# Optimization experiments

Measured on AMD Instinct MI355X. Metric: run time of the kernel, lower is better.

Reference implementation:

```python
import jax, jax.numpy as jnp
import numpy as np
from jax import lax

BETA = 0.95
THRESH = 1.0
NUM_INPUTS, NUM_HIDDEN, NUM_CLASSES, NUM_STEPS, BATCH = 80, 256, 2, 200, 4096


@jax.custom_vjp
def spike_fn(x):
    # Heaviside spike; surrogate gradient = fast_sigmoid (slope=25)
    return (x > 0).astype(x.dtype)

def _spike_fwd(x):
    return spike_fn(x), x

def _spike_bwd(x, g):
    slope = 25.0
    return (g / (slope * jnp.abs(x) + 1.0) ** 2,)

spike_fn.defvjp(_spike_fwd, _spike_bwd)


def _linear_init(key, fan_in, fan_out):
    # torch nn.Linear default init: U(-1/sqrt(fan_in), 1/sqrt(fan_in))
    k1, k2 = jax.random.split(key)
    bound = 1.0 / np.sqrt(fan_in)
    W = jax.random.uniform(k1, (fan_out, fan_in), jnp.float32, -bound, bound)
    b = jax.random.uniform(k2, (fan_out,), jnp.float32, -bound, bound)
    return W, b


def setup_inputs() -> dict:
    key = jax.random.key(0)
    kx, k1, k2, k3, k4 = jax.random.split(key, 5)
    x = jax.random.normal(kx, (BATCH, NUM_INPUTS, NUM_STEPS), jnp.float32)
    W1, b1 = _linear_init(k1, NUM_INPUTS, NUM_HIDDEN)
    W2, b2 = _linear_init(k2, NUM_HIDDEN, NUM_HIDDEN)
    W3, b3 = _linear_init(k3, NUM_HIDDEN, NUM_HIDDEN)
    W4, b4 = _linear_init(k4, NUM_HIDDEN, NUM_CLASSES)
    return {"x": x, "W1": W1, "b1": b1, "W2": W2, "b2": b2,
            "W3": W3, "b3": b3, "W4": W4, "b4": b4}


def _lif(cur, mem):
    # snntorch Leaky, reset_mechanism='subtract': reset from previous mem (detached)
    reset = lax.stop_gradient((mem > THRESH).astype(mem.dtype))
    mem = BETA * mem + cur - reset * THRESH
    spk = spike_fn(mem - THRESH)
    return spk, mem


def reference(x, W1, b1, W2, b2, W3, b3, W4, b4):
    B = x.shape[0]
    xt = jnp.transpose(x, (2, 0, 1))  # [T, B, 80]
    m1 = jnp.zeros((B, NUM_HIDDEN), x.dtype)
    m2 = jnp.zeros((B, NUM_HIDDEN), x.dtype)
    m3 = jnp.zeros((B, NUM_HIDDEN), x.dtype)
    m4 = jnp.zeros((B, NUM_CLASSES), x.dtype)

    def step(carry, x_t):
        m1, m2, m3, m4 = carry
        s1, m1 = _lif(x_t @ W1.T + b1, m1)
        s2, m2 = _lif(s1 @ W2.T + b2, m2)
        s3, m3 = _lif(s2 @ W3.T + b3, m3)
        s4, m4 = _lif(s3 @ W4.T + b4, m4)
        return (m1, m2, m3, m4), s4

    _, spk4_rec = lax.scan(step, (m1, m2, m3, m4), xt)
    return spk4_rec  # [T, B, num_classes]
```

## Files before the change

kernel.cpp:

```cpp
#include <hip/hip_runtime.h>
#include <cstddef>


#define BATCH 4096
#define TSTEPS 200
#define NIN 80
#define KP 96
#define NH 256
#define XPAD 104
#define SPAD 264

#define W1HI 0
#define W1LO 24576
#define W2HI 49152
#define W2LO 114688
#define W3HI 180224
#define W3LO 245760

#define LO_SCALE 2048.0f
#define LO_INV 4.8828125e-4f

typedef _Float16 h8 __attribute__((ext_vector_type(8)));
typedef float f4 __attribute__((ext_vector_type(4)));

__device__ __forceinline__ void lds_barrier() {
  __builtin_amdgcn_s_waitcnt(0xC07F);
  __builtin_amdgcn_s_barrier();
}

__device__ __forceinline__ void pin4(f4& v) { asm volatile("" : "+v"(v)); }

__global__ __launch_bounds__(256) void prep_kernel(
    const float* __restrict__ W1, const float* __restrict__ W2,
    const float* __restrict__ W3, _Float16* __restrict__ ws) {
  unsigned id = blockIdx.x * 256u + threadIdx.x;
  if (id >= 24576u + 65536u + 65536u) return;
  float v;
  unsigned off;
  _Float16 *hi, *lo;
  if (id < 24576u) {
    unsigned n = id / KP, k = id % KP;
    v = (k < NIN) ? W1[n * NIN + k] : 0.0f;
    hi = ws + W1HI; lo = ws + W1LO; off = id;
  } else if (id < 90112u) {
    off = id - 24576u; v = W2[off];
    hi = ws + W2HI; lo = ws + W2LO;
  } else {
    off = id - 90112u; v = W3[off];
    hi = ws + W3HI; lo = ws + W3LO;
  }
  _Float16 h = (_Float16)v;
  float r = (v - (float)h) * LO_SCALE;
  hi[off] = h;
  lo[off] = (_Float16)r;
}

__global__ __launch_bounds__(1024, 4) void snn_kernel(
    const float* __restrict__ x,
    const float* __restrict__ b1, const float* __restrict__ b2,
    const float* __restrict__ b3, const float* __restrict__ W4,
    const float* __restrict__ b4, const _Float16* __restrict__ ws,
    float* __restrict__ out) {
  __shared__ alignas(16) _Float16 xAhi[4][16][XPAD];
  __shared__ alignas(16) _Float16 xAlo[4][16][XPAD];
  __shared__ alignas(16) _Float16 S1[16][SPAD];
  __shared__ alignas(16) _Float16 S2[16][SPAD];
  __shared__ alignas(16) _Float16 S3[16][SPAD];

  const int tid = threadIdx.x;
  const int wave = tid >> 6;
  const int lane = tid & 63;
  const int n16 = lane & 15;
  const int kg = lane >> 4;
  const int wb = blockIdx.x << 4;
  const int nn = (wave << 4) + n16;

  const _Float16* w1h = ws + W1HI + nn * KP;
  const _Float16* w1l = ws + W1LO + nn * KP;
  const _Float16* w2l = ws + W2LO + nn * NH;
  const _Float16* w3l = ws + W3LO + nn * NH;

  const float bb1 = b1[nn], bb2 = b2[nn], bb3 = b3[nn];

  f4 w2hi_f[8], w3hi_f[8];
  {
    const float* w2h = (const float*)(ws + W2HI + nn * NH);
    const float* w3h = (const float*)(ws + W3HI + nn * NH);
#pragma unroll
    for (int kt = 0; kt < 8; ++kt) {
      w2hi_f[kt] = *(const f4*)(w2h + kt * 16 + kg * 4);
      w3hi_f[kt] = *(const f4*)(w3h + kt * 16 + kg * 4);
    }
#pragma unroll
    for (int kt = 0; kt < 8; ++kt) {
      pin4(w2hi_f[kt]);
      pin4(w3hi_f[kt]);
    }
  }

  const int j4 = lane >> 5;
  const int ks4 = (lane & 31) << 3;
  const float* w4p = W4 + j4 * NH + ks4;
  const float bb4 = b4[j4];

  float mem1[4] = {0.f, 0.f, 0.f, 0.f};
  float mem2[4] = {0.f, 0.f, 0.f, 0.f};
  float mem3[4] = {0.f, 0.f, 0.f, 0.f};
  float mem4 = 0.f;

  for (int t = 0; t < TSTEPS; ++t) {
    const int ph = t & 3;
    if (ph == 0) {
      for (unsigned e = (unsigned)tid; e < 16u * KP; e += 1024u) {
        unsigned m = e / KP, i = e % KP;
        f4 v = {0.f, 0.f, 0.f, 0.f};
        if (i < NIN)
          v = __builtin_nontemporal_load(
              (const f4*)(x + ((size_t)(wb + m) * NIN + i) * TSTEPS + t));
#pragma unroll
        for (int s = 0; s < 4; ++s) {
          float f = v[s];
          _Float16 h = (_Float16)f;
          xAhi[s][m][i] = h;
          xAlo[s][m][i] = (_Float16)((f - (float)h) * LO_SCALE);
        }
      }
      lds_barrier();
    }

    h8 wh[3], wl1[3];
#pragma unroll
    for (int kt = 0; kt < 3; ++kt) {
      wh[kt] = *(const h8*)(w1h + kt * 32 + kg * 8);
      wl1[kt] = *(const h8*)(w1l + kt * 32 + kg * 8);
    }
    h8 wl2[8];
#pragma unroll
    for (int kt = 0; kt < 8; ++kt)
      wl2[kt] = *(const h8*)(w2l + kt * 32 + kg * 8);

    f4 aH = {0.f, 0.f, 0.f, 0.f};
    f4 aL = {0.f, 0.f, 0.f, 0.f};
#pragma unroll
    for (int kt = 0; kt < 3; ++kt) {
      const int ko = kt * 32 + kg * 8;
      h8 ahi = *(const h8*)&xAhi[ph][n16][ko];
      h8 alo = *(const h8*)&xAlo[ph][n16][ko];
      aH = __builtin_amdgcn_mfma_f32_16x16x32_f16(ahi, wh[kt], aH, 0, 0, 0);
      aL = __builtin_amdgcn_mfma_f32_16x16x32_f16(alo, wh[kt], aL, 0, 0, 0);
      aL = __builtin_amdgcn_mfma_f32_16x16x32_f16(ahi, wl1[kt], aL, 0, 0, 0);
    }
#pragma unroll
    for (int r = 0; r < 4; ++r) {
      float cur = __fadd_rn(__fadd_rn(aH[r], __fmul_rn(aL[r], LO_INV)), bb1);
      float mo = mem1[r];
      float mn = __fsub_rn(__fadd_rn(__fmul_rn(0.95f, mo), cur),
                           (mo > 1.0f) ? 1.0f : 0.0f);
      mem1[r] = mn;
      S1[kg * 4 + r][nn] = (mn > 1.0f) ? (_Float16)1.0f : (_Float16)0.0f;
    }
    lds_barrier();

    aH = (f4){0.f, 0.f, 0.f, 0.f};
    aL = (f4){0.f, 0.f, 0.f, 0.f};
#pragma unroll
    for (int kt = 0; kt < 8; ++kt) {
      h8 a = *(const h8*)&S1[n16][kt * 32 + kg * 8];
      aH = __builtin_amdgcn_mfma_f32_16x16x32_f16(
          a, __builtin_bit_cast(h8, w2hi_f[kt]), aH, 0, 0, 0);
    }
#pragma unroll
    for (int kt = 0; kt < 8; ++kt) {
      h8 a = *(const h8*)&S1[n16][kt * 32 + kg * 8];
      aL = __builtin_amdgcn_mfma_f32_16x16x32_f16(a, wl2[kt], aL, 0, 0, 0);
    }
    h8 wl3[8];
#pragma unroll
    for (int kt = 0; kt < 8; ++kt)
      wl3[kt] = *(const h8*)(w3l + kt * 32 + kg * 8);
#pragma unroll
    for (int r = 0; r < 4; ++r) {
      float cur = __fadd_rn(__fadd_rn(aH[r], __fmul_rn(aL[r], LO_INV)), bb2);
      float mo = mem2[r];
      float mn = __fsub_rn(__fadd_rn(__fmul_rn(0.95f, mo), cur),
                           (mo > 1.0f) ? 1.0f : 0.0f);
      mem2[r] = mn;
      S2[kg * 4 + r][nn] = (mn > 1.0f) ? (_Float16)1.0f : (_Float16)0.0f;
    }
    lds_barrier();

    aH = (f4){0.f, 0.f, 0.f, 0.f};
    aL = (f4){0.f, 0.f, 0.f, 0.f};
#pragma unroll
    for (int kt = 0; kt < 8; ++kt) {
      h8 a = *(const h8*)&S2[n16][kt * 32 + kg * 8];
      aH = __builtin_amdgcn_mfma_f32_16x16x32_f16(
          a, __builtin_bit_cast(h8, w3hi_f[kt]), aH, 0, 0, 0);
    }
#pragma unroll
    for (int kt = 0; kt < 8; ++kt) {
      h8 a = *(const h8*)&S2[n16][kt * 32 + kg * 8];
      aL = __builtin_amdgcn_mfma_f32_16x16x32_f16(a, wl3[kt], aL, 0, 0, 0);
    }
    f4 w4a = *(const f4*)(w4p);
    f4 w4b = *(const f4*)(w4p + 4);
#pragma unroll
    for (int r = 0; r < 4; ++r) {
      float cur = __fadd_rn(__fadd_rn(aH[r], __fmul_rn(aL[r], LO_INV)), bb3);
      float mo = mem3[r];
      float mn = __fsub_rn(__fadd_rn(__fmul_rn(0.95f, mo), cur),
                           (mo > 1.0f) ? 1.0f : 0.0f);
      mem3[r] = mn;
      S3[kg * 4 + r][nn] = (mn > 1.0f) ? (_Float16)1.0f : (_Float16)0.0f;
    }
    lds_barrier();

    {
      h8 s = *(const h8*)&S3[wave][ks4];
      float p = 0.0f;
#pragma unroll
      for (int u = 0; u < 4; ++u)
        p = __fadd_rn(p, __fmul_rn((float)s[u], w4a[u]));
#pragma unroll
      for (int u = 0; u < 4; ++u)
        p = __fadd_rn(p, __fmul_rn((float)s[4 + u], w4b[u]));
#pragma unroll
      for (int msk = 1; msk <= 16; msk <<= 1)
        p = __fadd_rn(p, __shfl_xor(p, msk));
      float cur = __fadd_rn(p, bb4);
      float mo = mem4;
      float mn = __fsub_rn(__fadd_rn(__fmul_rn(0.95f, mo), cur),
                           (mo > 1.0f) ? 1.0f : 0.0f);
      mem4 = mn;
      if ((lane & 31) == 0)
        __builtin_nontemporal_store(
            (mn > 1.0f) ? 1.0f : 0.0f,
            out + (size_t)t * (BATCH * 2) + (size_t)(wb + wave) * 2 + j4);
    }
  }
}

extern "C" void kernel_launch(void* const* d_in, const int* in_sizes, int n_in,
                              void* d_out, int out_size, void* d_ws,
                              size_t ws_size, hipStream_t stream) {
  const float* x  = (const float*)d_in[0];
  const float* W1 = (const float*)d_in[1];
  const float* b1 = (const float*)d_in[2];
  const float* W2 = (const float*)d_in[3];
  const float* b2 = (const float*)d_in[4];
  const float* W3 = (const float*)d_in[5];
  const float* b3 = (const float*)d_in[6];
  const float* W4 = (const float*)d_in[7];
  const float* b4 = (const float*)d_in[8];
  float* out = (float*)d_out;
  _Float16* ws = (_Float16*)d_ws;

  hipLaunchKernelGGL(prep_kernel, dim3(608), dim3(256), 0, stream,
                     W1, W2, W3, ws);
  hipLaunchKernelGGL(snn_kernel, dim3(BATCH / 16), dim3(1024), 0, stream,
                     x, b1, b2, b3, W4, b4, ws, out);
}
```

Before: 3.041 ms.

## Stage W1 hi/lo weights in LDS and split low-weight prefetches into halves

Copies the W1 hi and lo fp16 tables (256x96 each) into shared memory once per block, so the per-step layer-1 weight reads come from LDS instead of global memory. Splits the per-step global prefetch of W2/W3 low-part weights into two halves issued at different points to shorten register live ranges and overlap loads with MFMA work. Replaces launch_bounds min-blocks with amdgpu_waves_per_eu(4,4). This adds about 106KB of LDS per block, which may cut occupancy, and the staging copy has no barrier before its first use. That is covered only indirectly by the later x-load barrier.

```diff
diff --git a/kernel.cpp b/kernel.cpp
--- a/kernel.cpp
+++ b/kernel.cpp
@@ -9,6 +9,7 @@
 #define NH 256
 #define XPAD 104
 #define SPAD 264
+#define WP1 104
 
 #define W1HI 0
 #define W1LO 24576
@@ -55,12 +56,15 @@
   lo[off] = (_Float16)r;
 }
 
-__global__ __launch_bounds__(1024, 4) void snn_kernel(
+__global__ __attribute__((amdgpu_waves_per_eu(4, 4)))
+__launch_bounds__(1024) void snn_kernel(
     const float* __restrict__ x,
     const float* __restrict__ b1, const float* __restrict__ b2,
     const float* __restrict__ b3, const float* __restrict__ W4,
     const float* __restrict__ b4, const _Float16* __restrict__ ws,
     float* __restrict__ out) {
+  __shared__ alignas(16) _Float16 Wh1[256][WP1];
+  __shared__ alignas(16) _Float16 Wl1[256][WP1];
   __shared__ alignas(16) _Float16 xAhi[4][16][XPAD];
   __shared__ alignas(16) _Float16 xAlo[4][16][XPAD];
   __shared__ alignas(16) _Float16 S1[16][SPAD];
@@ -75,8 +79,12 @@
   const int wb = blockIdx.x << 4;
   const int nn = (wave << 4) + n16;
 
-  const _Float16* w1h = ws + W1HI + nn * KP;
-  const _Float16* w1l = ws + W1LO + nn * KP;
+  for (int c = tid; c < 3072; c += 1024) {
+    int row = c / 12, w = c % 12;
+    *(h8*)&Wh1[row][w * 8] = *(const h8*)(ws + W1HI + row * KP + w * 8);
+    *(h8*)&Wl1[row][w * 8] = *(const h8*)(ws + W1LO + row * KP + w * 8);
+  }
+
   const _Float16* w2l = ws + W2LO + nn * NH;
   const _Float16* w3l = ws + W3LO + nn * NH;
 
@@ -128,16 +136,10 @@
       lds_barrier();
     }
 
-    h8 wh[3], wl1[3];
-#pragma unroll
-    for (int kt = 0; kt < 3; ++kt) {
-      wh[kt] = *(const h8*)(w1h + kt * 32 + kg * 8);
-      wl1[kt] = *(const h8*)(w1l + kt * 32 + kg * 8);
-    }
-    h8 wl2[8];
-#pragma unroll
-    for (int kt = 0; kt < 8; ++kt)
-      wl2[kt] = *(const h8*)(w2l + kt * 32 + kg * 8);
+    h8 wl2a[4];
+#pragma unroll
+    for (int q = 0; q < 4; ++q)
+      wl2a[q] = *(const h8*)(w2l + q * 32 + kg * 8);
 
     f4 aH = {0.f, 0.f, 0.f, 0.f};
     f4 aL = {0.f, 0.f, 0.f, 0.f};
@@ -146,9 +148,11 @@
       const int ko = kt * 32 + kg * 8;
       h8 ahi = *(const h8*)&xAhi[ph][n16][ko];
       h8 alo = *(const h8*)&xAlo[ph][n16][ko];
-      aH = __builtin_amdgcn_mfma_f32_16x16x32_f16(ahi, wh[kt], aH, 0, 0, 0);
-      aL = __builtin_amdgcn_mfma_f32_16x16x32_f16(alo, wh[kt], aL, 0, 0, 0);
-      aL = __builtin_amdgcn_mfma_f32_16x16x32_f16(ahi, wl1[kt], aL, 0, 0, 0);
+      h8 wh = *(const h8*)&Wh1[nn][ko];
+      h8 wl = *(const h8*)&Wl1[nn][ko];
+      aH = __builtin_amdgcn_mfma_f32_16x16x32_f16(ahi, wh, aH, 0, 0, 0);
+      aL = __builtin_amdgcn_mfma_f32_16x16x32_f16(alo, wh, aL, 0, 0, 0);
+      aL = __builtin_amdgcn_mfma_f32_16x16x32_f16(ahi, wl, aL, 0, 0, 0);
     }
 #pragma unroll
     for (int r = 0; r < 4; ++r) {
@@ -161,6 +165,11 @@
     }
     lds_barrier();
 
+    h8 wl2b[4];
+#pragma unroll
+    for (int q = 0; q < 4; ++q)
+      wl2b[q] = *(const h8*)(w2l + (4 + q) * 32 + kg * 8);
+
     aH = (f4){0.f, 0.f, 0.f, 0.f};
     aL = (f4){0.f, 0.f, 0.f, 0.f};
 #pragma unroll
@@ -170,14 +179,19 @@
           a, __builtin_bit_cast(h8, w2hi_f[kt]), aH, 0, 0, 0);
     }
 #pragma unroll
-    for (int kt = 0; kt < 8; ++kt) {
-      h8 a = *(const h8*)&S1[n16][kt * 32 + kg * 8];
-      aL = __builtin_amdgcn_mfma_f32_16x16x32_f16(a, wl2[kt], aL, 0, 0, 0);
-    }
-    h8 wl3[8];
-#pragma unroll
-    for (int kt = 0; kt < 8; ++kt)
-      wl3[kt] = *(const h8*)(w3l + kt * 32 + kg * 8);
+    for (int q = 0; q < 4; ++q) {
+      h8 a = *(const h8*)&S1[n16][q * 32 + kg * 8];
+      aL = __builtin_amdgcn_mfma_f32_16x16x32_f16(a, wl2a[q], aL, 0, 0, 0);
+    }
+    h8 wl3a[4];
+#pragma unroll
+    for (int q = 0; q < 4; ++q)
+      wl3a[q] = *(const h8*)(w3l + q * 32 + kg * 8);
+#pragma unroll
+    for (int q = 0; q < 4; ++q) {
+      h8 a = *(const h8*)&S1[n16][(4 + q) * 32 + kg * 8];
+      aL = __builtin_amdgcn_mfma_f32_16x16x32_f16(a, wl2b[q], aL, 0, 0, 0);
+    }
 #pragma unroll
     for (int r = 0; r < 4; ++r) {
       float cur = __fadd_rn(__fadd_rn(aH[r], __fmul_rn(aL[r], LO_INV)), bb2);
@@ -189,6 +203,11 @@
     }
     lds_barrier();
 
+    h8 wl3b[4];
+#pragma unroll
+    for (int q = 0; q < 4; ++q)
+      wl3b[q] = *(const h8*)(w3l + (4 + q) * 32 + kg * 8);
+
     aH = (f4){0.f, 0.f, 0.f, 0.f};
     aL = (f4){0.f, 0.f, 0.f, 0.f};
 #pragma unroll
@@ -198,12 +217,17 @@
           a, __builtin_bit_cast(h8, w3hi_f[kt]), aH, 0, 0, 0);
     }
 #pragma unroll
-    for (int kt = 0; kt < 8; ++kt) {
-      h8 a = *(const h8*)&S2[n16][kt * 32 + kg * 8];
-      aL = __builtin_amdgcn_mfma_f32_16x16x32_f16(a, wl3[kt], aL, 0, 0, 0);
+    for (int q = 0; q < 4; ++q) {
+      h8 a = *(const h8*)&S2[n16][q * 32 + kg * 8];
+      aL = __builtin_amdgcn_mfma_f32_16x16x32_f16(a, wl3a[q], aL, 0, 0, 0);
     }
     f4 w4a = *(const f4*)(w4p);
     f4 w4b = *(const f4*)(w4p + 4);
+#pragma unroll
+    for (int q = 0; q < 4; ++q) {
+      h8 a = *(const h8*)&S2[n16][(4 + q) * 32 + kg * 8];
+      aL = __builtin_amdgcn_mfma_f32_16x16x32_f16(a, wl3b[q], aL, 0, 0, 0);
+    }
 #pragma unroll
     for (int r = 0; r < 4; ++r) {
       float cur = __fadd_rn(__fadd_rn(aH[r], __fmul_rn(aL[r], LO_INV)), bb3);
```

Result: faster. 2.510 ms (-17.4%).
